# Kernel optimization log

Hardware: AMD Instinct MI355X
Metric: run time of the kernel (lower is better)

Reference implementation:

```python
import jax, jax.numpy as jnp
import numpy as np

N_HEAD = 16
N_KV = 4
HEAD_DIM = 128
WINDOW = 1024
SINK = 4
THETA = 10000.0


def _rope_cos_sin(T, dim, theta, dtype):
    inv_freq = 1.0 / (theta ** (jnp.arange(0, dim, 2, dtype=jnp.float32) / dim))
    t = jnp.arange(T, dtype=jnp.float32)
    ang = jnp.outer(t, inv_freq)  # [T, dim/2]
    return jnp.cos(ang).astype(dtype), jnp.sin(ang).astype(dtype)


def _apply_rope(x, cos, sin):
    # x: [B, H, T, D]; cos/sin: [T, D/2]
    d2 = x.shape[-1] // 2
    x1, x2 = x[..., :d2], x[..., d2:]
    return jnp.concatenate([x1 * cos - x2 * sin, x2 * cos + x1 * sin], axis=-1)


def setup_inputs() -> dict:
    key = jax.random.key(0)
    ks = jax.random.split(key, 5)
    B, T, C = 2, 2048, 2048
    x = jax.random.normal(ks[0], (B, T, C), dtype=jnp.float32)
    s = 0.02
    wq = jax.random.normal(ks[1], (C, C), dtype=jnp.float32) * s
    wk = jax.random.normal(ks[2], (N_KV * HEAD_DIM, C), dtype=jnp.float32) * s
    wv = jax.random.normal(ks[3], (N_KV * HEAD_DIM, C), dtype=jnp.float32) * s
    wo = jax.random.normal(ks[4], (C, C), dtype=jnp.float32) * s
    return {"x": x, "wq": wq, "wk": wk, "wv": wv, "wo": wo}


def reference(x, wq, wk, wv, wo):
    B, T, C = x.shape
    # QKV projections (Linear with weight [out, in], no bias)
    q = (x @ wq.T).reshape(B, T, N_HEAD, HEAD_DIM).transpose(0, 2, 1, 3)  # [B,H,T,D]
    k = (x @ wk.T).reshape(B, T, N_KV, HEAD_DIM).transpose(0, 2, 1, 3)    # [B,Hkv,T,D]
    v = (x @ wv.T).reshape(B, T, N_KV, HEAD_DIM).transpose(0, 2, 1, 3)

    cos, sin = _rope_cos_sin(T, HEAD_DIM, THETA, x.dtype)
    q = _apply_rope(q, cos, sin)
    k = _apply_rope(k, cos, sin)

    # GQA: repeat kv heads to match query heads (repeat_interleave on head dim)
    rep = N_HEAD // N_KV
    k = jnp.repeat(k, rep, axis=1)
    v = jnp.repeat(v, rep, axis=1)

    # causal + sliding window + attention sink mask
    i = jnp.arange(T)[:, None]
    j = jnp.arange(T)[None, :]
    allowed = (j <= i) & (((i - j) <= WINDOW) | (j < SINK))
    bias = jnp.where(allowed, 0.0, -jnp.inf).astype(x.dtype)  # [T,T]

    scale = 1.0 / np.sqrt(HEAD_DIM)
    att = jnp.einsum("bhqd,bhkd->bhqk", q, k) * scale + bias
    att = jax.nn.softmax(att, axis=-1)
    y = jnp.einsum("bhqk,bhkd->bhqd", att, v)  # [B,H,T,D]
    y = y.transpose(0, 2, 1, 3).reshape(B, T, C)
    return y @ wo.T
```

## Files before the change

kernel.cpp:

```cpp
#include <hip/hip_runtime.h>
#include <hip/hip_bf16.h>

typedef __bf16 bf16x8 __attribute__((ext_vector_type(8)));
typedef __bf16 bf16x4 __attribute__((ext_vector_type(4)));
typedef float  f32x4  __attribute__((ext_vector_type(4)));
typedef float  f32x16 __attribute__((ext_vector_type(16)));
typedef unsigned int uint4v __attribute__((ext_vector_type(4)));

#define NB     2
#define TT     2048
#define CC     2048
#define NH     16
#define NKV    4
#define HD     128
#define WIN    1024
#define SINKN  4
#define QSCALE2 (0.08838834764831845f * 1.44269504088896340f)

__device__ __forceinline__ void lds_load16(const void* g, void* l) {
    __builtin_amdgcn_global_load_lds(
        (__attribute__((address_space(1))) void*)const_cast<void*>(g),
        (__attribute__((address_space(3))) void*)l, 16, 0, 0);
}

__device__ __forceinline__ unsigned pack2bf(float a, float b) {
    __bf16 x = (__bf16)a, y = (__bf16)b;
    unsigned short ux = __builtin_bit_cast(unsigned short, x);
    unsigned short uy = __builtin_bit_cast(unsigned short, y);
    return (unsigned)ux | ((unsigned)uy << 16);
}

__device__ __forceinline__ float fast_exp2(float x) {
    float r;
    asm("v_exp_f32 %0, %1" : "=v"(r) : "v"(x));
    return r;
}

__global__ void prolog_kernel(const float* __restrict__ x,
                              const float* __restrict__ wq, const float* __restrict__ wk,
                              const float* __restrict__ wv, const float* __restrict__ wo,
                              __bf16* __restrict__ xb, __bf16* __restrict__ Wall,
                              float* __restrict__ cosT, float* __restrict__ sinT) {
    const int g = blockIdx.x * 256 + threadIdx.x;
    if (g < 2097152) {
        const int idx = g * 4;
        const float4 v = *(const float4*)(x + idx);
        bf16x4 o;
        o[0] = (__bf16)v.x; o[1] = (__bf16)v.y; o[2] = (__bf16)v.z; o[3] = (__bf16)v.w;
        *(bf16x4*)(xb + idx) = o;
    } else if (g < 4718592) {
        const int idx = (g - 2097152) * 4;
        const float* src; int off;
        if (idx < 4194304)      { src = wq; off = idx; }
        else if (idx < 5242880) { src = wk; off = idx - 4194304; }
        else if (idx < 6291456) { src = wv; off = idx - 5242880; }
        else                    { src = wo; off = idx - 6291456; }
        const float4 v = *(const float4*)(src + off);
        bf16x4 o;
        o[0] = (__bf16)v.x; o[1] = (__bf16)v.y; o[2] = (__bf16)v.z; o[3] = (__bf16)v.w;
        *(bf16x4*)(Wall + idx) = o;
    } else {
        const int i = g - 4718592;
        const int t = i >> 6, d = i & 63;
        const float inv_freq = 1.0f / powf(10000.0f, (float)d * (1.0f / 64.0f));
        const float ang = (float)t * inv_freq;
        cosT[i] = cosf(ang);
        sinT[i] = sinf(ang);
    }
}

__global__ void scatter_vt_kernel(const __bf16* __restrict__ qkv,
                                  const float* __restrict__ cosT,
                                  const float* __restrict__ sinT,
                                  __bf16* __restrict__ Qo,
                                  __bf16* __restrict__ Ko,
                                  __bf16* __restrict__ Vt) {
    __shared__ __bf16 tile[64][72];
    if (blockIdx.x < 2560) {
        const int job = blockIdx.x * 256 + threadIdx.x;
        int m, d8, base_off; __bf16* outp; float scale;
        if (job < 524288) {
            m = job >> 7;
            const int pj = job & 127;
            const int hh = pj >> 3; d8 = pj & 7;
            base_off = hh * 128;
            const int b = m >> 11, t = m & 2047;
            outp = Qo + ((size_t)(b * NH + hh) * TT + t) * HD + d8 * 8;
            scale = QSCALE2;
        } else {
            const int j2 = job - 524288;
            m = j2 >> 5;
            const int pj = j2 & 31;
            const int g = pj >> 3; d8 = pj & 7;
            base_off = 2048 + g * 128;
            const int b = m >> 11, t = m & 2047;
            outp = Ko + ((size_t)(b * NKV + g) * TT + t) * HD + d8 * 8;
            scale = 1.0f;
        }
        const int t = m & 2047;
        const __bf16* row = qkv + (size_t)m * 3072 + base_off + d8 * 8;
        const bf16x8 x1 = *(const bf16x8*)row;
        const bf16x8 x2 = *(const bf16x8*)(row + 64);
        const float4 c0 = *(const float4*)(cosT + t * 64 + d8 * 8);
        const float4 c1 = *(const float4*)(cosT + t * 64 + d8 * 8 + 4);
        const float4 s0 = *(const float4*)(sinT + t * 64 + d8 * 8);
        const float4 s1 = *(const float4*)(sinT + t * 64 + d8 * 8 + 4);
        const float cs[8] = {c0.x, c0.y, c0.z, c0.w, c1.x, c1.y, c1.z, c1.w};
        const float sn[8] = {s0.x, s0.y, s0.z, s0.w, s1.x, s1.y, s1.z, s1.w};
        bf16x8 o1, o2;
#pragma unroll
        for (int e = 0; e < 8; ++e) {
            const float a = (float)x1[e], bb = (float)x2[e];
            o1[e] = (__bf16)((a * cs[e] - bb * sn[e]) * scale);
            o2[e] = (__bf16)((bb * cs[e] + a * sn[e]) * scale);
        }
        *(bf16x8*)outp = o1;
        *(bf16x8*)(outp + 64) = o2;
    } else {
        const int idx2 = blockIdx.x - 2560;
        const int t0 = (idx2 & 31) << 6, d0 = ((idx2 >> 5) & 1) << 6, bkv = idx2 >> 6;
        const int b = bkv >> 2, g = bkv & 3;
        const int r = threadIdx.x >> 2, cg = threadIdx.x & 3;
        const __bf16* src = qkv + (size_t)(b * TT + t0 + r) * 3072 + 2560 + g * 128 + d0 + cg * 16;
        *(bf16x8*)&tile[r][cg * 16]     = *(const bf16x8*)src;
        *(bf16x8*)&tile[r][cg * 16 + 8] = *(const bf16x8*)(src + 8);
        __syncthreads();
        __bf16* dst = Vt + ((size_t)bkv * HD + d0 + r) * TT + t0 + cg * 16;
        bf16x8 o0, o1;
#pragma unroll
        for (int c2 = 0; c2 < 8; ++c2) {
            o0[c2] = tile[cg * 16 + c2][r];
            o1[c2] = tile[cg * 16 + 8 + c2][r];
        }
        *(bf16x8*)dst = o0;
        *(bf16x8*)(dst + 8) = o1;
    }
}

template <int OUT_BF16>
__global__ __launch_bounds__(512, 2) void gemm_bt8(const __bf16* __restrict__ A,
                                                   const __bf16* __restrict__ Bm,
                                                   void* __restrict__ C,
                                                   int M, int N, int K) {
    __shared__ __align__(16) __bf16 lA[2][256 * 64];
    __shared__ __align__(16) __bf16 lB[2][192 * 64];
    const int tid = threadIdx.x;
    const int lane = tid & 63;
    const int w = tid >> 6;
    const int wm = w >> 2, wn = w & 3;
    const int nbn = N / 192;
    const int nwg = (M >> 8) * nbn;
    const int chunk = nwg >> 3;
    const int swz = (blockIdx.x & 7) * chunk + (blockIdx.x >> 3);
    const int bm = swz / nbn, bn = swz % nbn;
    const int m0 = bm << 8, n0 = bn * 192;
    const int lr = lane & 15, lh = lane >> 4;
    const int NT = K >> 6;

    auto stageA = [&](int kt, int buf, int i) {
        const int d = i * 8192 + tid * 16;
        const int row = d >> 7;
        const int colb = (d & 127) ^ ((row & 7) << 4);
        lds_load16(A + (size_t)(m0 + row) * K + kt * 64 + (colb >> 1),
                   (char*)lA[buf] + i * 8192 + w * 1024);
    };
    auto stageB = [&](int kt, int buf, int i) {
        const int d = i * 8192 + tid * 16;
        const int row = d >> 7;
        const int colb = (d & 127) ^ ((row & 7) << 4);
        lds_load16(Bm + (size_t)(n0 + row) * K + kt * 64 + (colb >> 1),
                   (char*)lB[buf] + i * 8192 + w * 1024);
    };

    f32x4 acc[8][3] = {};

#pragma unroll
    for (int i = 0; i < 4; ++i) stageA(0, 0, i);
#pragma unroll
    for (int i = 0; i < 3; ++i) stageB(0, 0, i);
    asm volatile("s_waitcnt vmcnt(0)" ::: "memory");
    __syncthreads();

    for (int kt = 0; kt < NT; ++kt) {
        const int cur = kt & 1, nxt = cur ^ 1;
        const bool pf = (kt + 1 < NT);
        const char* bA = (const char*)lA[cur];
        const char* bB = (const char*)lB[cur];

        bf16x8 aF[4][2], bf3[3][2];
#pragma unroll
        for (int mf = 0; mf < 4; ++mf)
#pragma unroll
            for (int ks = 0; ks < 2; ++ks) {
                const int row = wm * 128 + mf * 16 + lr;
                const int cb = (ks * 64 + lh * 16) ^ ((row & 7) << 4);
                aF[mf][ks] = *(const bf16x8*)(bA + row * 128 + cb);
            }
#pragma unroll
        for (int nf = 0; nf < 3; ++nf)
#pragma unroll
            for (int ks = 0; ks < 2; ++ks) {
                const int row = wn * 48 + nf * 16 + lr;
                const int cb = (ks * 64 + lh * 16) ^ ((row & 7) << 4);
                bf3[nf][ks] = *(const bf16x8*)(bB + row * 128 + cb);
            }
        if (pf) { stageA(kt + 1, nxt, 0); stageA(kt + 1, nxt, 1); stageA(kt + 1, nxt, 2); stageA(kt + 1, nxt, 3); }
        __builtin_amdgcn_s_setprio(1);
#pragma unroll
        for (int mf = 0; mf < 4; ++mf)
#pragma unroll
            for (int nf = 0; nf < 3; ++nf)
#pragma unroll
                for (int ks = 0; ks < 2; ++ks)
                    acc[mf][nf] = __builtin_amdgcn_mfma_f32_16x16x32_bf16(aF[mf][ks], bf3[nf][ks], acc[mf][nf], 0, 0, 0);
        __builtin_amdgcn_s_setprio(0);

#pragma unroll
        for (int mf = 0; mf < 4; ++mf)
#pragma unroll
            for (int ks = 0; ks < 2; ++ks) {
                const int row = wm * 128 + 64 + mf * 16 + lr;
                const int cb = (ks * 64 + lh * 16) ^ ((row & 7) << 4);
                aF[mf][ks] = *(const bf16x8*)(bA + row * 128 + cb);
            }
        if (pf) { stageB(kt + 1, nxt, 0); stageB(kt + 1, nxt, 1); stageB(kt + 1, nxt, 2); }
        __builtin_amdgcn_s_setprio(1);
#pragma unroll
        for (int mf = 0; mf < 4; ++mf)
#pragma unroll
            for (int nf = 0; nf < 3; ++nf)
#pragma unroll
                for (int ks = 0; ks < 2; ++ks)
                    acc[mf + 4][nf] = __builtin_amdgcn_mfma_f32_16x16x32_bf16(aF[mf][ks], bf3[nf][ks], acc[mf + 4][nf], 0, 0, 0);
        __builtin_amdgcn_s_setprio(0);

        asm volatile("s_waitcnt vmcnt(0)" ::: "memory");
        __syncthreads();
    }

#pragma unroll
    for (int mf = 0; mf < 8; ++mf)
#pragma unroll
        for (int nf = 0; nf < 3; ++nf)
#pragma unroll
            for (int r = 0; r < 4; ++r) {
                const size_t row = m0 + wm * 128 + mf * 16 + lh * 4 + r;
                const size_t col = n0 + wn * 48 + nf * 16 + lr;
                if (OUT_BF16) ((__bf16*)C)[row * N + col] = (__bf16)acc[mf][nf][r];
                else          ((float*)C)[row * N + col]  = acc[mf][nf][r];
            }
}

template <int OUT_BF16>
__global__ __launch_bounds__(256, 2) void gemm_bt(const __bf16* __restrict__ A,
                                                  const __bf16* __restrict__ Bm,
                                                  void* __restrict__ C,
                                                  int M, int N, int K) {
    __shared__ __align__(16) __bf16 lA[2][128 * 64];
    __shared__ __align__(16) __bf16 lB[2][128 * 64];
    const int tid = threadIdx.x;
    const int lane = tid & 63;
    const int w = tid >> 6;
    const int wr = w >> 1, wc = w & 1;
    const int nbn = N >> 7;
    const int nwg = (M >> 7) * nbn;
    const int chunk = nwg >> 3;
    const int swz = (blockIdx.x & 7) * chunk + (blockIdx.x >> 3);
    const int bm = swz / nbn, bn = swz % nbn;
    const int m0 = bm << 7, n0 = bn << 7;
    const int lr = lane & 15, lh = lane >> 4;
    f32x4 acc[4][4] = {};

    auto stage = [&](int k0, int buf) {
#pragma unroll
        for (int i = 0; i < 4; ++i) {
            const int d = i * 4096 + tid * 16;
            const int row = d >> 7;
            const int colb = (d & 127) ^ ((row & 7) << 4);
            lds_load16(A + (size_t)(m0 + row) * K + k0 + (colb >> 1),
                       (char*)lA[buf] + i * 4096 + w * 1024);
            lds_load16(Bm + (size_t)(n0 + row) * K + k0 + (colb >> 1),
                       (char*)lB[buf] + i * 4096 + w * 1024);
        }
    };

    stage(0, 0);
    asm volatile("s_waitcnt vmcnt(0)" ::: "memory");
    __syncthreads();

    const int NT = K >> 6;
    for (int kt = 0; kt < NT; ++kt) {
        const int buf = kt & 1;
        if (kt + 1 < NT) stage((kt + 1) << 6, buf ^ 1);

        const char* bA = (const char*)lA[buf];
        const char* bB = (const char*)lB[buf];
        bf16x8 af[4][2], bfr[4][2];
#pragma unroll
        for (int t = 0; t < 4; ++t)
#pragma unroll
            for (int ks = 0; ks < 2; ++ks) {
                const int rowa = wr * 64 + t * 16 + lr;
                const int cba = (ks * 64 + lh * 16) ^ ((rowa & 7) << 4);
                af[t][ks] = *(const bf16x8*)(bA + rowa * 128 + cba);
                const int rowb = wc * 64 + t * 16 + lr;
                const int cbb = (ks * 64 + lh * 16) ^ ((rowb & 7) << 4);
                bfr[t][ks] = *(const bf16x8*)(bB + rowb * 128 + cbb);
            }
#pragma unroll
        for (int mt = 0; mt < 4; ++mt)
#pragma unroll
            for (int nt = 0; nt < 4; ++nt)
#pragma unroll
                for (int ks = 0; ks < 2; ++ks)
                    acc[mt][nt] = __builtin_amdgcn_mfma_f32_16x16x32_bf16(af[mt][ks], bfr[nt][ks], acc[mt][nt], 0, 0, 0);

        asm volatile("s_waitcnt vmcnt(0)" ::: "memory");
        __syncthreads();
    }

    const int r0 = (lane >> 4) * 4;
#pragma unroll
    for (int mt = 0; mt < 4; ++mt)
#pragma unroll
        for (int nt = 0; nt < 4; ++nt)
#pragma unroll
            for (int r = 0; r < 4; ++r) {
                const size_t row = m0 + wr * 64 + mt * 16 + r0 + r;
                const size_t col = n0 + wc * 64 + nt * 16 + lr;
                if (OUT_BF16) ((__bf16*)C)[row * N + col] = (__bf16)acc[mt][nt][r];
                else          ((float*)C)[row * N + col]  = acc[mt][nt][r];
            }
}

__global__ __launch_bounds__(256, 2) void attn_kernel(const __bf16* __restrict__ Q,
                                                      const __bf16* __restrict__ Kg,
                                                      const __bf16* __restrict__ Vt,
                                                      __bf16* __restrict__ Y) {
    const int id = blockIdx.x;
    const int grp = id & 7;
    const int pos = id >> 3;
    const int kv = grp & 3, b = grp >> 2;
    const int qt2 = 63 - pos;
    const int q0 = qt2 << 5;
    const int tid = threadIdx.x, lane = tid & 63, w = tid >> 6;
    const int l31 = lane & 31, hi = lane >> 5;
    const int h  = kv * 4 + w;

    __shared__ __align__(16) __bf16 lK[64 * 128];
    __shared__ __align__(16) __bf16 lV[128 * 64];

    bf16x8 qf[8];
    {
        const __bf16* Qb = Q + ((size_t)(b * NH + h) * TT + q0) * HD;
#pragma unroll
        for (int c = 0; c < 8; ++c)
            qf[c] = *(const bf16x8*)(Qb + l31 * HD + c * 16 + hi * 8);
    }

    f32x16 acc[4] = {};
    float mrun = -1e30f, lrun = 0.f;
    const int iq = q0 + l31;

    const __bf16* Kb = Kg + (size_t)(b * NKV + kv) * TT * HD;
    const __bf16* Vb = Vt + (size_t)(b * NKV + kv) * HD * TT;
    const int jend = qt2 >> 1;
    const int jsw  = (q0 > WIN) ? ((q0 - WIN) >> 6) : 0;

    for (int jb = 0; jb <= jend; ++jb) {
        if (jb > 0 && jb < jsw) continue;
        const int j0 = jb << 6;
        __syncthreads();
#pragma unroll
        for (int i = 0; i < 4; ++i) {
            const int o = i * 4096 + tid * 16;
            {
                const int row = o >> 8;
                const int colb = (o & 255) ^ ((row & 7) << 4);
                lds_load16(Kb + (size_t)(j0 + row) * HD + (colb >> 1),
                           (char*)lK + i * 4096 + w * 1024);
            }
            {
                const int row = o >> 7;
                const int colb = (o & 127) ^ ((row & 7) << 4);
                lds_load16(Vb + (size_t)row * TT + j0 + (colb >> 1),
                           (char*)lV + i * 4096 + w * 1024);
            }
        }
        asm volatile("s_waitcnt vmcnt(0)" ::: "memory");
        __syncthreads();

        f32x16 st[2];
#pragma unroll
        for (int kt2 = 0; kt2 < 2; ++kt2) {
            f32x16 s = {};
#pragma unroll
            for (int c = 0; c < 8; ++c) {
                const int row = kt2 * 32 + l31;
                const int cb = (c * 32 + hi * 16) ^ ((row & 7) << 4);
                const bf16x8 kf = *(const bf16x8*)((const char*)lK + row * 256 + cb);
                s = __builtin_amdgcn_mfma_f32_32x32x16_bf16(kf, qf[c], s, 0, 0, 0);
            }
            st[kt2] = s;
        }

        const bool fullTile = (j0 + 63 <= q0) && (q0 + 31 - j0 <= WIN);
        if (!fullTile) {
#pragma unroll
            for (int kt2 = 0; kt2 < 2; ++kt2)
#pragma unroll
                for (int rr = 0; rr < 16; ++rr) {
                    const int j = j0 + kt2 * 32 + (rr & 3) + 8 * (rr >> 2) + 4 * hi;
                    const bool ok = (j <= iq) && ((iq - j <= WIN) || (j < SINKN));
                    if (!ok) st[kt2][rr] = -1e30f;
                }
        }

        float mx = st[0][0];
#pragma unroll
        for (int kt2 = 0; kt2 < 2; ++kt2)
#pragma unroll
            for (int rr = 0; rr < 16; ++rr) mx = fmaxf(mx, st[kt2][rr]);
        mx = fmaxf(mx, __shfl_xor(mx, 32, 64));

        if (!__all(mx - mrun <= 11.53f)) {
            const float mnew = fmaxf(mrun, mx);
            const float corr = fast_exp2(mrun - mnew);
            mrun = mnew;
            lrun *= corr;
#pragma unroll
            for (int rr = 0; rr < 16; ++rr) {
                const float cq = __shfl(corr, (rr & 3) + 8 * (rr >> 2) + 4 * hi, 64);
#pragma unroll
                for (int dt = 0; dt < 4; ++dt) acc[dt][rr] *= cq;
            }
        }

        float rsum = 0.f;
#pragma unroll
        for (int kt2 = 0; kt2 < 2; ++kt2)
#pragma unroll
            for (int rr = 0; rr < 16; ++rr) {
                const float p = fast_exp2(st[kt2][rr] - mrun);
                st[kt2][rr] = p;
                rsum += p;
            }
        rsum += __shfl_xor(rsum, 32, 64);
        lrun += rsum;

        bf16x8 pa[4];
#pragma unroll
        for (int c = 0; c < 4; ++c) {
            const int kt2 = c >> 1, g = c & 1, base = 8 * g;
            const unsigned u1a = pack2bf(st[kt2][base + 0], st[kt2][base + 1]);
            const unsigned u1b = pack2bf(st[kt2][base + 2], st[kt2][base + 3]);
            const unsigned u2a = pack2bf(st[kt2][base + 4], st[kt2][base + 5]);
            const unsigned u2b = pack2bf(st[kt2][base + 6], st[kt2][base + 7]);
            const unsigned p1a = (unsigned)__shfl_xor((int)u1a, 32, 64);
            const unsigned p1b = (unsigned)__shfl_xor((int)u1b, 32, 64);
            const unsigned p2a = (unsigned)__shfl_xor((int)u2a, 32, 64);
            const unsigned p2b = (unsigned)__shfl_xor((int)u2b, 32, 64);
            uint4v uv;
            uv[0] = hi ? p2a : u1a;
            uv[1] = hi ? p2b : u1b;
            uv[2] = hi ? u2a : p1a;
            uv[3] = hi ? u2b : p1b;
            pa[c] = __builtin_bit_cast(bf16x8, uv);
        }

#pragma unroll
        for (int dt = 0; dt < 4; ++dt) {
            const int row = dt * 32 + l31;
            const int swzr = (row & 7) << 4;
#pragma unroll
            for (int c = 0; c < 4; ++c) {
                const int cb = (c * 32 + hi * 16) ^ swzr;
                const bf16x8 vf = *(const bf16x8*)((const char*)lV + row * 128 + cb);
                acc[dt] = __builtin_amdgcn_mfma_f32_32x32x16_bf16(pa[c], vf, acc[dt], 0, 0, 0);
            }
        }
    }

    const float inv = 1.f / lrun;
    float invq[16];
#pragma unroll
    for (int rr = 0; rr < 16; ++rr)
        invq[rr] = __shfl(inv, (rr & 3) + 8 * (rr >> 2) + 4 * hi, 64);
#pragma unroll
    for (int dt = 0; dt < 4; ++dt)
#pragma unroll
        for (int rr = 0; rr < 16; ++rr) {
            const int qrow = (rr & 3) + 8 * (rr >> 2) + 4 * hi;
            Y[((size_t)b * TT + q0 + qrow) * CC + h * HD + dt * 32 + l31] =
                (__bf16)(acc[dt][rr] * invq[rr]);
        }
}

extern "C" void kernel_launch(void* const* d_in, const int* in_sizes, int n_in,
                              void* d_out, int out_size, void* d_ws, size_t ws_size,
                              hipStream_t stream) {
    const float* x  = (const float*)d_in[0];
    const float* wq = (const float*)d_in[1];
    const float* wk = (const float*)d_in[2];
    const float* wv = (const float*)d_in[3];
    const float* wo = (const float*)d_in[4];
    float* out = (float*)d_out;

    char* ws = (char*)d_ws;
    size_t off = 0;
    auto alloc = [&](size_t bytes) { char* p = ws + off; off += bytes; return p; };
    __bf16* xb   = (__bf16*)alloc(16777216);
    __bf16* Wall = (__bf16*)alloc(12582912);
    __bf16* wob  = (__bf16*)alloc(8388608);
    __bf16* qkv  = (__bf16*)alloc(25165824);
    __bf16* Qs   = (__bf16*)alloc(16777216);
    __bf16* Ks   = (__bf16*)alloc(4194304);
    __bf16* Vts  = (__bf16*)alloc(4194304);
    float*  cosT = (float*)alloc(524288);
    float*  sinT = (float*)alloc(524288);
    __bf16* Yb = xb;

    prolog_kernel<<<18944, 256, 0, stream>>>(x, wq, wk, wv, wo, xb, Wall, cosT, sinT);
    gemm_bt8<1><<<dim3(256), 512, 0, stream>>>(xb, Wall, qkv, 4096, 3072, 2048);
    scatter_vt_kernel<<<3072, 256, 0, stream>>>(qkv, cosT, sinT, Qs, Ks, Vts);
    attn_kernel<<<dim3(512), 256, 0, stream>>>(Qs, Ks, Vts, Yb);
    gemm_bt<0><<<dim3(32 * 16), 256, 0, stream>>>(Yb, wob, out, 4096, 2048, 2048);
}
```

Before: 158.9 us.

## Use triple-buffered LDS pipeline and 256x128 tiles in QKV GEMM

The QKV projection GEMM goes from 256x192 tiles with double buffering to 256x128 tiles with a three-stage LDS ring. Loads are issued two k-steps ahead, and a partial vmcnt wait replaces the full drain before each barrier. The launch grows from 256 to 384 workgroups, which gives better coverage of the compute units and more load/compute overlap. In exchange, each tile does less reuse per loaded byte, and the kernel uses more LDS (about 144KB), which may limit it to one workgroup per CU.

```diff
diff --git a/kernel.cpp b/kernel.cpp
--- a/kernel.cpp
+++ b/kernel.cpp
@@ -142,52 +142,54 @@
                                                    const __bf16* __restrict__ Bm,
                                                    void* __restrict__ C,
                                                    int M, int N, int K) {
-    __shared__ __align__(16) __bf16 lA[2][256 * 64];
-    __shared__ __align__(16) __bf16 lB[2][192 * 64];
+    __shared__ __align__(16) __bf16 lA[3][256 * 64];
+    __shared__ __align__(16) __bf16 lB[3][128 * 64];
     const int tid = threadIdx.x;
     const int lane = tid & 63;
     const int w = tid >> 6;
     const int wm = w >> 2, wn = w & 3;
-    const int nbn = N / 192;
+    const int nbn = N >> 7;
     const int nwg = (M >> 8) * nbn;
     const int chunk = nwg >> 3;
     const int swz = (blockIdx.x & 7) * chunk + (blockIdx.x >> 3);
     const int bm = swz / nbn, bn = swz % nbn;
-    const int m0 = bm << 8, n0 = bn * 192;
+    const int m0 = bm << 8, n0 = bn << 7;
     const int lr = lane & 15, lh = lane >> 4;
     const int NT = K >> 6;
 
-    auto stageA = [&](int kt, int buf, int i) {
-        const int d = i * 8192 + tid * 16;
-        const int row = d >> 7;
-        const int colb = (d & 127) ^ ((row & 7) << 4);
-        lds_load16(A + (size_t)(m0 + row) * K + kt * 64 + (colb >> 1),
-                   (char*)lA[buf] + i * 8192 + w * 1024);
+    auto stageT = [&](int kt, int buf) {
+#pragma unroll
+        for (int i = 0; i < 4; ++i) {
+            const int d = i * 8192 + tid * 16;
+            const int row = d >> 7;
+            const int colb = (d & 127) ^ ((row & 7) << 4);
+            lds_load16(A + (size_t)(m0 + row) * K + kt * 64 + (colb >> 1),
+                       (char*)lA[buf] + i * 8192 + w * 1024);
+        }
+#pragma unroll
+        for (int i = 0; i < 2; ++i) {
+            const int d = i * 8192 + tid * 16;
+            const int row = d >> 7;
+            const int colb = (d & 127) ^ ((row & 7) << 4);
+            lds_load16(Bm + (size_t)(n0 + row) * K + kt * 64 + (colb >> 1),
+                       (char*)lB[buf] + i * 8192 + w * 1024);
+        }
     };
-    auto stageB = [&](int kt, int buf, int i) {
-        const int d = i * 8192 + tid * 16;
-        const int row = d >> 7;
-        const int colb = (d & 127) ^ ((row & 7) << 4);
-        lds_load16(Bm + (size_t)(n0 + row) * K + kt * 64 + (colb >> 1),
-                   (char*)lB[buf] + i * 8192 + w * 1024);
-    };
-
-    f32x4 acc[8][3] = {};
-
-#pragma unroll
-    for (int i = 0; i < 4; ++i) stageA(0, 0, i);
-#pragma unroll
-    for (int i = 0; i < 3; ++i) stageB(0, 0, i);
-    asm volatile("s_waitcnt vmcnt(0)" ::: "memory");
-    __syncthreads();
+
+    f32x4 acc[8][2] = {};
+
+    stageT(0, 0);
+    stageT(1, 1);
+    asm volatile("s_waitcnt vmcnt(6)" ::: "memory");
+    __builtin_amdgcn_s_barrier();
+    __builtin_amdgcn_sched_barrier(0);
 
     for (int kt = 0; kt < NT; ++kt) {
-        const int cur = kt & 1, nxt = cur ^ 1;
-        const bool pf = (kt + 1 < NT);
+        const int cur = kt % 3;
         const char* bA = (const char*)lA[cur];
         const char* bB = (const char*)lB[cur];
 
-        bf16x8 aF[4][2], bf3[3][2];
+        bf16x8 aF[4][2], bf2[2][2];
 #pragma unroll
         for (int mf = 0; mf < 4; ++mf)
 #pragma unroll
@@ -197,22 +199,22 @@
                 aF[mf][ks] = *(const bf16x8*)(bA + row * 128 + cb);
             }
 #pragma unroll
-        for (int nf = 0; nf < 3; ++nf)
+        for (int nf = 0; nf < 2; ++nf)
 #pragma unroll
             for (int ks = 0; ks < 2; ++ks) {
-                const int row = wn * 48 + nf * 16 + lr;
+                const int row = wn * 32 + nf * 16 + lr;
                 const int cb = (ks * 64 + lh * 16) ^ ((row & 7) << 4);
-                bf3[nf][ks] = *(const bf16x8*)(bB + row * 128 + cb);
-            }
-        if (pf) { stageA(kt + 1, nxt, 0); stageA(kt + 1, nxt, 1); stageA(kt + 1, nxt, 2); stageA(kt + 1, nxt, 3); }
+                bf2[nf][ks] = *(const bf16x8*)(bB + row * 128 + cb);
+            }
+        if (kt + 2 < NT) stageT(kt + 2, (kt + 2) % 3);
         __builtin_amdgcn_s_setprio(1);
 #pragma unroll
         for (int mf = 0; mf < 4; ++mf)
 #pragma unroll
-            for (int nf = 0; nf < 3; ++nf)
+            for (int nf = 0; nf < 2; ++nf)
 #pragma unroll
                 for (int ks = 0; ks < 2; ++ks)
-                    acc[mf][nf] = __builtin_amdgcn_mfma_f32_16x16x32_bf16(aF[mf][ks], bf3[nf][ks], acc[mf][nf], 0, 0, 0);
+                    acc[mf][nf] = __builtin_amdgcn_mfma_f32_16x16x32_bf16(aF[mf][ks], bf2[nf][ks], acc[mf][nf], 0, 0, 0);
         __builtin_amdgcn_s_setprio(0);
 
 #pragma unroll
@@ -223,29 +225,30 @@
                 const int cb = (ks * 64 + lh * 16) ^ ((row & 7) << 4);
                 aF[mf][ks] = *(const bf16x8*)(bA + row * 128 + cb);
             }
-        if (pf) { stageB(kt + 1, nxt, 0); stageB(kt + 1, nxt, 1); stageB(kt + 1, nxt, 2); }
         __builtin_amdgcn_s_setprio(1);
 #pragma unroll
         for (int mf = 0; mf < 4; ++mf)
 #pragma unroll
-            for (int nf = 0; nf < 3; ++nf)
+            for (int nf = 0; nf < 2; ++nf)
 #pragma unroll
                 for (int ks = 0; ks < 2; ++ks)
-                    acc[mf + 4][nf] = __builtin_amdgcn_mfma_f32_16x16x32_bf16(aF[mf][ks], bf3[nf][ks], acc[mf + 4][nf], 0, 0, 0);
+                    acc[mf + 4][nf] = __builtin_amdgcn_mfma_f32_16x16x32_bf16(aF[mf][ks], bf2[nf][ks], acc[mf + 4][nf], 0, 0, 0);
         __builtin_amdgcn_s_setprio(0);
 
-        asm volatile("s_waitcnt vmcnt(0)" ::: "memory");
-        __syncthreads();
+        if (kt + 2 < NT) asm volatile("s_waitcnt vmcnt(6)" ::: "memory");
+        else             asm volatile("s_waitcnt vmcnt(0)" ::: "memory");
+        __builtin_amdgcn_s_barrier();
+        __builtin_amdgcn_sched_barrier(0);
     }
 
 #pragma unroll
     for (int mf = 0; mf < 8; ++mf)
 #pragma unroll
-        for (int nf = 0; nf < 3; ++nf)
+        for (int nf = 0; nf < 2; ++nf)
 #pragma unroll
             for (int r = 0; r < 4; ++r) {
                 const size_t row = m0 + wm * 128 + mf * 16 + lh * 4 + r;
-                const size_t col = n0 + wn * 48 + nf * 16 + lr;
+                const size_t col = n0 + wn * 32 + nf * 16 + lr;
                 if (OUT_BF16) ((__bf16*)C)[row * N + col] = (__bf16)acc[mf][nf][r];
                 else          ((float*)C)[row * N + col]  = acc[mf][nf][r];
             }
@@ -521,7 +524,7 @@
     __bf16* Yb = xb;
 
     prolog_kernel<<<18944, 256, 0, stream>>>(x, wq, wk, wv, wo, xb, Wall, cosT, sinT);
-    gemm_bt8<1><<<dim3(256), 512, 0, stream>>>(xb, Wall, qkv, 4096, 3072, 2048);
+    gemm_bt8<1><<<dim3(384), 512, 0, stream>>>(xb, Wall, qkv, 4096, 3072, 2048);
     scatter_vt_kernel<<<3072, 256, 0, stream>>>(qkv, cosT, sinT, Qs, Ks, Vts);
     attn_kernel<<<dim3(512), 256, 0, stream>>>(Qs, Ks, Vts, Yb);
     gemm_bt<0><<<dim3(32 * 16), 256, 0, stream>>>(Yb, wob, out, 4096, 2048, 2048);
```

New measurement: 190.1 us. 19.6% more time.

## Double-buffer K/V tiles in attention kernel to overlap loads with MFMA

Applied to the files above, without the earlier changes.

Attention K/V LDS tiles are now double-buffered. The next tile is prefetched via global_load_lds while the current one is being computed, and a partial vmcnt wait lets the prefetch stay in flight. The iteration over kept blocks is rewritten as an explicit list (sink block followed by the window blocks), so no loop iterations are skipped via continue. This doubles LDS use to 64KB per block, which may reduce occupancy below the launch bound of 2 blocks per CU, and it depends on manual barrier placement for correctness.

```diff
diff --git a/kernel.cpp b/kernel.cpp
--- a/kernel.cpp
+++ b/kernel.cpp
@@ -347,8 +347,8 @@
     const int l31 = lane & 31, hi = lane >> 5;
     const int h  = kv * 4 + w;
 
-    __shared__ __align__(16) __bf16 lK[64 * 128];
-    __shared__ __align__(16) __bf16 lV[128 * 64];
+    __shared__ __align__(16) __bf16 lK[2][64 * 128];
+    __shared__ __align__(16) __bf16 lV[2][128 * 64];
 
     bf16x8 qf[8];
     {
@@ -366,29 +366,45 @@
     const __bf16* Vb = Vt + (size_t)(b * NKV + kv) * HD * TT;
     const int jend = qt2 >> 1;
     const int jsw  = (q0 > WIN) ? ((q0 - WIN) >> 6) : 0;
-
-    for (int jb = 0; jb <= jend; ++jb) {
-        if (jb > 0 && jb < jsw) continue;
-        const int j0 = jb << 6;
-        __syncthreads();
+    const int jswe = (jsw < 1) ? 1 : jsw;
+    const int nv   = (jend >= jswe) ? (jend - jswe + 2) : 1;
+
+    auto stage = [&](int jb, int buf) {
+        const int j0s = jb << 6;
 #pragma unroll
         for (int i = 0; i < 4; ++i) {
             const int o = i * 4096 + tid * 16;
             {
                 const int row = o >> 8;
                 const int colb = (o & 255) ^ ((row & 7) << 4);
-                lds_load16(Kb + (size_t)(j0 + row) * HD + (colb >> 1),
-                           (char*)lK + i * 4096 + w * 1024);
+                lds_load16(Kb + (size_t)(j0s + row) * HD + (colb >> 1),
+                           (char*)lK[buf] + i * 4096 + w * 1024);
             }
             {
                 const int row = o >> 7;
                 const int colb = (o & 127) ^ ((row & 7) << 4);
-                lds_load16(Vb + (size_t)row * TT + j0 + (colb >> 1),
-                           (char*)lV + i * 4096 + w * 1024);
-            }
-        }
-        asm volatile("s_waitcnt vmcnt(0)" ::: "memory");
-        __syncthreads();
+                lds_load16(Vb + (size_t)row * TT + j0s + (colb >> 1),
+                           (char*)lV[buf] + i * 4096 + w * 1024);
+            }
+        }
+    };
+
+    stage(0, 0);
+
+    for (int idx = 0; idx < nv; ++idx) {
+        const int cur = idx & 1;
+        const bool pf = (idx + 1 < nv);
+        const int jb = (idx == 0) ? 0 : (jswe + idx - 1);
+        const int j0 = jb << 6;
+
+        if (pf) stage(jswe + idx, cur ^ 1);
+        if (pf) asm volatile("s_waitcnt vmcnt(8)" ::: "memory");
+        else    asm volatile("s_waitcnt vmcnt(0)" ::: "memory");
+        __builtin_amdgcn_s_barrier();
+        __builtin_amdgcn_sched_barrier(0);
+
+        const char* bK = (const char*)lK[cur];
+        const char* bV = (const char*)lV[cur];
 
         f32x16 st[2];
 #pragma unroll
@@ -398,7 +414,7 @@
             for (int c = 0; c < 8; ++c) {
                 const int row = kt2 * 32 + l31;
                 const int cb = (c * 32 + hi * 16) ^ ((row & 7) << 4);
-                const bf16x8 kf = *(const bf16x8*)((const char*)lK + row * 256 + cb);
+                const bf16x8 kf = *(const bf16x8*)(bK + row * 256 + cb);
                 s = __builtin_amdgcn_mfma_f32_32x32x16_bf16(kf, qf[c], s, 0, 0, 0);
             }
             st[kt2] = s;
@@ -475,10 +491,12 @@
 #pragma unroll
             for (int c = 0; c < 4; ++c) {
                 const int cb = (c * 32 + hi * 16) ^ swzr;
-                const bf16x8 vf = *(const bf16x8*)((const char*)lV + row * 128 + cb);
+                const bf16x8 vf = *(const bf16x8*)(bV + row * 128 + cb);
                 acc[dt] = __builtin_amdgcn_mfma_f32_32x32x16_bf16(pa[c], vf, acc[dt], 0, 0, 0);
             }
         }
+
+        if (pf) __builtin_amdgcn_s_barrier();
     }
 
     const float inv = 1.f / lrun;
```

After: 158.6 us. Within noise of the previous version (-0.2%).
